# Kernel optimization log

Measured on AMD Instinct MI355X. Metric: run time of the kernel, lower is better.

Reference implementation:

```python
import jax, jax.numpy as jnp
import numpy as np
from math import log2, ceil

NUM_LEAVES = 128
KERNEL = 8
STRIDE = 8
PADDING = 0
LR = 0.3

LEAF_NUM = 2 ** ceil(log2(NUM_LEAVES))   # 128
DEPTH = int(log2(LEAF_NUM))              # 7
NUM_NODES = 2 * LEAF_NUM - 1             # 255


def _ancestor_table():
    # A[j-1, t-1] = global heap index of the ancestor of node j at tree level t,
    # or -1 if t exceeds j's own level. Nodes use heap indexing: children of i
    # are 2i+1, 2i+2 (matches the layer bookkeeping in the torch module).
    A = np.full((NUM_NODES - 1, DEPTH), -1, dtype=np.int32)
    for j in range(1, NUM_NODES):
        lvl = int(np.floor(np.log2(j + 1)))
        anc = j
        for t in range(lvl, 0, -1):
            A[j - 1, t - 1] = anc
            anc = (anc - 1) // 2
    return jnp.asarray(A)

_ANC = _ancestor_table()  # (NUM_NODES-1, DEPTH)


def img2patches(x):
    x = jnp.pad(x, PADDING)
    H, W = x.shape
    n0 = (H - KERNEL) // STRIDE + 1
    n1 = (W - KERNEL) // STRIDE + 1
    win = jnp.arange(KERNEL)
    rows = jnp.arange(n0)[:, None] * STRIDE + win[None, :]  # (n0, k)
    cols = jnp.arange(n1)[:, None] * STRIDE + win[None, :]  # (n1, k)
    p = x[rows[:, None, :, None], cols[None, :, None, :]]   # (n0, n1, k, k)
    return p.reshape(n0 * n1, KERNEL * KERNEL)


def setup_inputs() -> dict:
    key = jax.random.key(0)
    k1, k2 = jax.random.split(key)
    image = jax.random.uniform(k1, (2048, 2048), dtype=jnp.float32)
    nodes = jax.random.uniform(k2, (NUM_NODES, KERNEL * KERNEL), dtype=jnp.float32)
    return {"image": image, "nodes": nodes}


def reference(image, nodes):
    X = img2patches(image)                      # (P, k^2)
    P = X.shape[0]

    # --- hierarchical BMU descent (binary tree, DEPTH levels) ---
    cur = jnp.zeros((P,), dtype=jnp.int32)      # root
    bmu_levels = []
    for _ in range(DEPTH):
        c0 = 2 * cur + 1
        c1 = 2 * cur + 2
        # pnorm with p=2 in the source is (sum((a-b)^2))^2 -- monotone, kept faithful
        d0 = jnp.sum((nodes[c0] - X) ** 2, axis=-1) ** 2
        d1 = jnp.sum((nodes[c1] - X) ** 2, axis=-1) ** 2
        cur = jnp.where(d1 < d0, c1, c0)        # tie -> first (c0), like torch.min
        bmu_levels.append(cur)
    bmu_path = jnp.stack(bmu_levels, axis=1)    # (P, DEPTH), bmu at levels 1..DEPTH

    # --- layer_state for every non-root node: number of levels at which the
    # node's ancestor coincides with the BMU chain (== the torch concatenated
    # layer_state, columns ordered by global node index 1..NUM_NODES-1) ---
    state = jnp.sum(_ANC[None, :, :] == bmu_path[:, None, :], axis=-1)  # (P, N-1)

    lrates = LR * (2.0 ** jnp.arange(1, DEPTH + 2, dtype=jnp.float32)) / 2.0 ** (DEPTH + 1)
    lrs = lrates[state]                          # (P, N-1)

    # mean_p lrs[p,j] * (X[p,:] - nodes[1+j,:])
    #   = (lrs^T @ X)/P - mean_p(lrs)[:,None] * nodes[1:]
    upd = jnp.einsum('pj,pk->jk', lrs, X) / P - lrs.mean(axis=0)[:, None] * nodes[1:]
    new_nodes = nodes.at[1:].add(upd)

    return new_nodes, cur[:, None]               # updated codebook, leaf BMU per patch
```

## Files before the change

kernel.cpp:

```cpp
#include <hip/hip_runtime.h>

#define IMG_W 2048
#define NUM_NODES 255
#define NLEAF 128
#define DEPTH 7
#define RS 68

template<int CTRL>
__device__ __forceinline__ float dpp_add(float x) {
    int v = __builtin_amdgcn_update_dpp(0, __float_as_int(x), CTRL, 0xF, 0xF, true);
    return x + __int_as_float(v);
}
__device__ __forceinline__ float group16_sum(float x) {
    x = dpp_add<0xB1>(x);
    x = dpp_add<0x4E>(x);
    x = dpp_add<0x141>(x);
    x = dpp_add<0x128>(x);
    return x;
}

__global__ __launch_bounds__(1024, 4) void fusedK(const float* __restrict__ img,
                                                  const float* __restrict__ nodes,
                                                  float* __restrict__ leaf_out,
                                                  float* __restrict__ S,
                                                  unsigned* __restrict__ cnt)
{
    __shared__ float nds[NUM_NODES * RS];
    __shared__ float Sl[NLEAF * RS];
    __shared__ unsigned cntl[NLEAF];

    const int t = threadIdx.x;
    const int b = blockIdx.x;
    const int g = t >> 4;
    const int q = t & 15;
    const int q4 = q * 4;

    float4 xv0, xv1, xv2, xv3;
    {
        const int roff = (q >> 1), coff = (q & 1) * 4;
        int p = b * 256 + g;
        xv0 = *(const float4*)(img + (size_t)((p >> 8) * 8 + roff) * IMG_W + (p & 255) * 8 + coff);
        p += 64;
        xv1 = *(const float4*)(img + (size_t)((p >> 8) * 8 + roff) * IMG_W + (p & 255) * 8 + coff);
        p += 64;
        xv2 = *(const float4*)(img + (size_t)((p >> 8) * 8 + roff) * IMG_W + (p & 255) * 8 + coff);
        p += 64;
        xv3 = *(const float4*)(img + (size_t)((p >> 8) * 8 + roff) * IMG_W + (p & 255) * 8 + coff);
    }

    for (int i = t; i < NLEAF * RS; i += 1024) Sl[i] = 0.0f;
    if (t < NLEAF) cntl[t] = 0u;

    const float4* ng = (const float4*)nodes;
    for (int i = t; i < NUM_NODES * 16; i += 1024) {
        *(float4*)&nds[(i >> 4) * RS + (i & 15) * 4] = ng[i];
    }
    __syncthreads();

    int cur0 = 0, cur1 = 0, cur2 = 0, cur3 = 0;
    #pragma unroll
    for (int lvl = 0; lvl < DEPTH; ++lvl) {
        const int ca = 2 * cur0 + 1, cb = 2 * cur1 + 1, cc = 2 * cur2 + 1, cd = 2 * cur3 + 1;
        const float* pa = &nds[ca * RS + q4];
        const float* pb = &nds[cb * RS + q4];
        const float* pc = &nds[cc * RS + q4];
        const float* pd = &nds[cd * RS + q4];
        const float4 A0 = *(const float4*)(pa);
        const float4 B0 = *(const float4*)(pa + RS);
        const float4 A1 = *(const float4*)(pb);
        const float4 B1 = *(const float4*)(pb + RS);
        const float4 A2 = *(const float4*)(pc);
        const float4 B2 = *(const float4*)(pc + RS);
        const float4 A3 = *(const float4*)(pd);
        const float4 B3 = *(const float4*)(pd + RS);

        float d, s0, s1;
        s0 = 0.f; s1 = 0.f;
        d = A0.x - xv0.x; s0 = fmaf(d, d, s0);  d = B0.x - xv0.x; s1 = fmaf(d, d, s1);
        d = A0.y - xv0.y; s0 = fmaf(d, d, s0);  d = B0.y - xv0.y; s1 = fmaf(d, d, s1);
        d = A0.z - xv0.z; s0 = fmaf(d, d, s0);  d = B0.z - xv0.z; s1 = fmaf(d, d, s1);
        d = A0.w - xv0.w; s0 = fmaf(d, d, s0);  d = B0.w - xv0.w; s1 = fmaf(d, d, s1);
        cur0 = (group16_sum(s1 - s0) < 0.0f) ? (ca + 1) : ca;
        s0 = 0.f; s1 = 0.f;
        d = A1.x - xv1.x; s0 = fmaf(d, d, s0);  d = B1.x - xv1.x; s1 = fmaf(d, d, s1);
        d = A1.y - xv1.y; s0 = fmaf(d, d, s0);  d = B1.y - xv1.y; s1 = fmaf(d, d, s1);
        d = A1.z - xv1.z; s0 = fmaf(d, d, s0);  d = B1.z - xv1.z; s1 = fmaf(d, d, s1);
        d = A1.w - xv1.w; s0 = fmaf(d, d, s0);  d = B1.w - xv1.w; s1 = fmaf(d, d, s1);
        cur1 = (group16_sum(s1 - s0) < 0.0f) ? (cb + 1) : cb;
        s0 = 0.f; s1 = 0.f;
        d = A2.x - xv2.x; s0 = fmaf(d, d, s0);  d = B2.x - xv2.x; s1 = fmaf(d, d, s1);
        d = A2.y - xv2.y; s0 = fmaf(d, d, s0);  d = B2.y - xv2.y; s1 = fmaf(d, d, s1);
        d = A2.z - xv2.z; s0 = fmaf(d, d, s0);  d = B2.z - xv2.z; s1 = fmaf(d, d, s1);
        d = A2.w - xv2.w; s0 = fmaf(d, d, s0);  d = B2.w - xv2.w; s1 = fmaf(d, d, s1);
        cur2 = (group16_sum(s1 - s0) < 0.0f) ? (cc + 1) : cc;
        s0 = 0.f; s1 = 0.f;
        d = A3.x - xv3.x; s0 = fmaf(d, d, s0);  d = B3.x - xv3.x; s1 = fmaf(d, d, s1);
        d = A3.y - xv3.y; s0 = fmaf(d, d, s0);  d = B3.y - xv3.y; s1 = fmaf(d, d, s1);
        d = A3.z - xv3.z; s0 = fmaf(d, d, s0);  d = B3.z - xv3.z; s1 = fmaf(d, d, s1);
        d = A3.w - xv3.w; s0 = fmaf(d, d, s0);  d = B3.w - xv3.w; s1 = fmaf(d, d, s1);
        cur3 = (group16_sum(s1 - s0) < 0.0f) ? (cd + 1) : cd;
    }

    if (q == 0) {
        leaf_out[b * 256 + g]       = (float)cur0;
        leaf_out[b * 256 + 64 + g]  = (float)cur1;
        leaf_out[b * 256 + 128 + g] = (float)cur2;
        leaf_out[b * 256 + 192 + g] = (float)cur3;
        atomicAdd(&cntl[cur0 - 127], 1u);
        atomicAdd(&cntl[cur1 - 127], 1u);
        atomicAdd(&cntl[cur2 - 127], 1u);
        atomicAdd(&cntl[cur3 - 127], 1u);
    }

    {
        float* dst = &Sl[(cur0 - 127) * RS + q4];
        atomicAdd(dst + 0, xv0.x); atomicAdd(dst + 1, xv0.y);
        atomicAdd(dst + 2, xv0.z); atomicAdd(dst + 3, xv0.w);
        dst = &Sl[(cur1 - 127) * RS + q4];
        atomicAdd(dst + 0, xv1.x); atomicAdd(dst + 1, xv1.y);
        atomicAdd(dst + 2, xv1.z); atomicAdd(dst + 3, xv1.w);
        dst = &Sl[(cur2 - 127) * RS + q4];
        atomicAdd(dst + 0, xv2.x); atomicAdd(dst + 1, xv2.y);
        atomicAdd(dst + 2, xv2.z); atomicAdd(dst + 3, xv2.w);
        dst = &Sl[(cur3 - 127) * RS + q4];
        atomicAdd(dst + 0, xv3.x); atomicAdd(dst + 1, xv3.y);
        atomicAdd(dst + 2, xv3.z); atomicAdd(dst + 3, xv3.w);
    }
    __syncthreads();

    for (int i = t; i < NLEAF * 64; i += 1024) {
        const int row = i >> 6;
        if (cntl[row] == 0u) continue;
        const float v = Sl[row * RS + (i & 63)];
        if (v != 0.0f) atomicAdd(&S[i], v);
    }
    if (t < NLEAF && cntl[t] != 0u) atomicAdd(&cnt[t], cntl[t]);
}

__global__ __launch_bounds__(256) void updateK(const float* __restrict__ nodes,
                                               const float* __restrict__ S,
                                               const unsigned* __restrict__ cnt,
                                               float* __restrict__ out)
{
    const int gid = blockIdx.x * 256 + threadIdx.x;
    if (gid >= NUM_NODES * 64) return;
    const int n = gid >> 6, k = gid & 63;
    const float nd = nodes[gid];
    if (n == 0) { out[gid] = nd; return; }

    const int pos = n + 1;
    const int Ln = 31 - __clz(pos);
    float su = 0.f, sc = 0.f;
    #pragma unroll 8
    for (int L = 0; L < NLEAF; ++L) {
        const int a = (128 + L) >> (7 - Ln);
        const int x = pos ^ a;
        const int state = (x == 0) ? Ln : (Ln - (31 - __clz(x)) - 1);
        const float lr = 0.3f * ((float)(1 << state) * (1.0f / 128.0f));
        su = fmaf(lr, S[L * 64 + k], su);
        sc = fmaf(lr, (float)cnt[L], sc);
    }
    const float invP = 1.0f / 65536.0f;
    out[gid] = nd + su * invP - (sc * invP) * nd;
}

extern "C" void kernel_launch(void* const* d_in, const int* in_sizes, int n_in,
                              void* d_out, int out_size, void* d_ws, size_t ws_size,
                              hipStream_t stream)
{
    const float* img   = (const float*)d_in[0];
    const float* nodes = (const float*)d_in[1];

    float* out_nodes = (float*)d_out;
    float* out_leaf  = out_nodes + NUM_NODES * 64;

    float*    S   = (float*)d_ws;
    unsigned* cnt = (unsigned*)(S + NLEAF * 64);

    hipMemsetAsync(d_ws, 0, (NLEAF * 64) * sizeof(float) + NLEAF * sizeof(unsigned), stream);
    fusedK<<<256, 1024, 0, stream>>>(img, nodes, out_leaf, S, cnt);
    updateK<<<64, 256, 0, stream>>>(nodes, S, cnt, out_nodes);
}
```

Before: 108.9 us.

## Fuse memset, BMU kernel and update kernel into one cooperative launch

Removes the workspace memset and the separate update kernel by launching the fused kernel cooperatively. Grid-wide syncs order the in-kernel zeroing of S/cnt, the atomic accumulation, and the final node update. This saves two launches and their inter-kernel gaps, at the cost of two grid barriers and a requirement that all 256 blocks of 1024 threads be co-resident. The first grid.sync also replaces the block barrier that guarded the shared-memory node load.

```diff
diff --git a/kernel.cpp b/kernel.cpp
--- a/kernel.cpp
+++ b/kernel.cpp
@@ -1,4 +1,7 @@
 #include <hip/hip_runtime.h>
+#include <hip/hip_cooperative_groups.h>
+
+namespace cg = cooperative_groups;
 
 #define IMG_W 2048
 #define NUM_NODES 255
@@ -23,7 +26,8 @@
                                                   const float* __restrict__ nodes,
                                                   float* __restrict__ leaf_out,
                                                   float* __restrict__ S,
-                                                  unsigned* __restrict__ cnt)
+                                                  unsigned* __restrict__ cnt,
+                                                  float* __restrict__ out_nodes)
 {
     __shared__ float nds[NUM_NODES * RS];
     __shared__ float Sl[NLEAF * RS];
@@ -31,9 +35,15 @@
 
     const int t = threadIdx.x;
     const int b = blockIdx.x;
+    const int gid = b * 1024 + t;
     const int g = t >> 4;
     const int q = t & 15;
     const int q4 = q * 4;
+
+    cg::grid_group grid = cg::this_grid();
+
+    if (gid < NLEAF * 64) S[gid] = 0.0f;
+    if (gid < NLEAF) cnt[gid] = 0u;
 
     float4 xv0, xv1, xv2, xv3;
     {
@@ -55,7 +65,8 @@
     for (int i = t; i < NUM_NODES * 16; i += 1024) {
         *(float4*)&nds[(i >> 4) * RS + (i & 15) * 4] = ng[i];
     }
-    __syncthreads();
+
+    grid.sync();
 
     int cur0 = 0, cur1 = 0, cur2 = 0, cur3 = 0;
     #pragma unroll
@@ -135,33 +146,31 @@
         if (v != 0.0f) atomicAdd(&S[i], v);
     }
     if (t < NLEAF && cntl[t] != 0u) atomicAdd(&cnt[t], cntl[t]);
-}
 
-__global__ __launch_bounds__(256) void updateK(const float* __restrict__ nodes,
-                                               const float* __restrict__ S,
-                                               const unsigned* __restrict__ cnt,
-                                               float* __restrict__ out)
-{
-    const int gid = blockIdx.x * 256 + threadIdx.x;
-    if (gid >= NUM_NODES * 64) return;
-    const int n = gid >> 6, k = gid & 63;
-    const float nd = nodes[gid];
-    if (n == 0) { out[gid] = nd; return; }
+    grid.sync();
 
-    const int pos = n + 1;
-    const int Ln = 31 - __clz(pos);
-    float su = 0.f, sc = 0.f;
-    #pragma unroll 8
-    for (int L = 0; L < NLEAF; ++L) {
-        const int a = (128 + L) >> (7 - Ln);
-        const int x = pos ^ a;
-        const int state = (x == 0) ? Ln : (Ln - (31 - __clz(x)) - 1);
-        const float lr = 0.3f * ((float)(1 << state) * (1.0f / 128.0f));
-        su = fmaf(lr, S[L * 64 + k], su);
-        sc = fmaf(lr, (float)cnt[L], sc);
+    if (gid < NUM_NODES * 64) {
+        const int n = gid >> 6, k = gid & 63;
+        const float nd = nodes[gid];
+        if (n == 0) {
+            out_nodes[gid] = nd;
+        } else {
+            const int pos = n + 1;
+            const int Ln = 31 - __clz(pos);
+            float su = 0.f, sc = 0.f;
+            #pragma unroll 8
+            for (int L = 0; L < NLEAF; ++L) {
+                const int a = (128 + L) >> (7 - Ln);
+                const int x = pos ^ a;
+                const int state = (x == 0) ? Ln : (Ln - (31 - __clz(x)) - 1);
+                const float lr = 0.3f * ((float)(1 << state) * (1.0f / 128.0f));
+                su = fmaf(lr, S[L * 64 + k], su);
+                sc = fmaf(lr, (float)cnt[L], sc);
+            }
+            const float invP = 1.0f / 65536.0f;
+            out_nodes[gid] = nd + su * invP - (sc * invP) * nd;
+        }
     }
-    const float invP = 1.0f / 65536.0f;
-    out[gid] = nd + su * invP - (sc * invP) * nd;
 }
 
 extern "C" void kernel_launch(void* const* d_in, const int* in_sizes, int n_in,
@@ -177,7 +186,8 @@
     float*    S   = (float*)d_ws;
     unsigned* cnt = (unsigned*)(S + NLEAF * 64);
 
-    hipMemsetAsync(d_ws, 0, (NLEAF * 64) * sizeof(float) + NLEAF * sizeof(unsigned), stream);
-    fusedK<<<256, 1024, 0, stream>>>(img, nodes, out_leaf, S, cnt);
-    updateK<<<64, 256, 0, stream>>>(nodes, S, cnt, out_nodes);
+    void* args[] = { (void*)&img, (void*)&nodes, (void*)&out_leaf,
+                     (void*)&S, (void*)&cnt, (void*)&out_nodes };
+    hipLaunchCooperativeKernel((const void*)fusedK, dim3(256), dim3(1024),
+                               args, 0, stream);
 }
```

After: 167.0 us. 53.3% more time.
